# Kernel optimization log

Measured on AMD Instinct MI355X. Metric: run time of the kernel, lower is better.

## Reference

```python
import jax, jax.numpy as jnp
import numpy as np

V = 100000  # node_num
N = 2000000  # number of rows/messages
D = 64       # feature dim


def setup_inputs() -> dict:
    key = jax.random.key(0)
    k1, k2 = jax.random.split(key)
    H = jax.random.normal(k1, (N, D), dtype=jnp.float32)
    X_node = jax.random.randint(k2, (N,), 0, V, dtype=jnp.int64)
    return {"H": H, "X_node": X_node}


def reference(H, X_node):
    # Original builds a [V, N] one-hot mask (mask[v, n] = 1 iff X_node[n] == v)
    # and computes mask @ H. That is exactly a segment-sum of H rows by node id.
    return jax.ops.segment_sum(H, X_node, num_segments=V)  # [V, D]
```

## Files before the change

kernel.cpp:

```cpp
#include <hip/hip_runtime.h>


constexpr int D = 64;
constexpr int SCAN_TILE = 1024;

__global__ void hist_kernel(const int* __restrict__ idx, int* __restrict__ hist, int N) {
    int stride = gridDim.x * blockDim.x;
    for (int n = blockIdx.x * blockDim.x + threadIdx.x; n < N; n += stride)
        atomicAdd(&hist[idx[n]], 1);
}

__global__ __launch_bounds__(1024) void scan_tile_kernel(
    const int* __restrict__ hist, int* __restrict__ starts,
    int* __restrict__ tile_sums, int V)
{
    __shared__ int tmp[SCAN_TILE];
    int t = threadIdx.x;
    int v = blockIdx.x * SCAN_TILE + t;
    int x = (v < V) ? hist[v] : 0;
    tmp[t] = x;
    __syncthreads();
    for (int off = 1; off < SCAN_TILE; off <<= 1) {
        int y = (t >= off) ? tmp[t - off] : 0;
        __syncthreads();
        tmp[t] += y;
        __syncthreads();
    }
    if (v < V) starts[v] = tmp[t] - x;
    if (t == SCAN_TILE - 1) tile_sums[blockIdx.x] = tmp[t];
}

__global__ void scan_sums_kernel(int* tile_sums, int n_tiles) {
    if (threadIdx.x == 0 && blockIdx.x == 0) {
        int run = 0;
        for (int i = 0; i < n_tiles; ++i) { int s = tile_sums[i]; tile_sums[i] = run; run += s; }
    }
}

__global__ __launch_bounds__(1024) void scan_add_kernel(
    int* __restrict__ starts, const int* __restrict__ tile_sums, int V)
{
    int v = blockIdx.x * SCAN_TILE + threadIdx.x;
    if (v < V) starts[v] += tile_sums[blockIdx.x];
}

__global__ void scatter_kernel(const int* __restrict__ idx, int* __restrict__ cursor,
                               int* __restrict__ perm, int N)
{
    int stride = gridDim.x * blockDim.x;
    for (int n = blockIdx.x * blockDim.x + threadIdx.x; n < N; n += stride) {
        int node = idx[n];
        int pos = atomicAdd(&cursor[node], 1);
        perm[pos] = n;
    }
}

__global__ __launch_bounds__(256) void gather_kernel(
    const float* __restrict__ H, const int* __restrict__ perm,
    const int* __restrict__ starts, float* __restrict__ out, int V, int N)
{
    int wid  = blockIdx.x * (blockDim.x >> 6) + (threadIdx.x >> 6);
    int lane = threadIdx.x & 63;
    if (wid >= V) return;

    int beg = starts[wid];
    int end = (wid + 1 < V) ? starts[wid + 1] : N;
    int cnt = end - beg;

    float acc = 0.f;
    int base = 0;
    while (base < cnt) {
        int m = cnt - base; if (m > 64) m = 64;
        int n_l = (lane < m) ? perm[beg + base + lane] : 0;
        int i = 0;
        for (; i + 3 < m; i += 4) {
            int n0 = __shfl(n_l, i);
            int n1 = __shfl(n_l, i + 1);
            int n2 = __shfl(n_l, i + 2);
            int n3 = __shfl(n_l, i + 3);
            float a0 = H[(size_t)n0 * D + lane];
            float a1 = H[(size_t)n1 * D + lane];
            float a2 = H[(size_t)n2 * D + lane];
            float a3 = H[(size_t)n3 * D + lane];
            acc += a0; acc += a1; acc += a2; acc += a3;
        }
        for (; i < m; ++i) {
            int n = __shfl(n_l, i);
            acc += H[(size_t)n * D + lane];
        }
        base += m;
    }
    out[(size_t)wid * D + lane] = acc;
}

__global__ __launch_bounds__(256) void scatter_atomic_kernel(
    const float4* __restrict__ H4, const int* __restrict__ idx,
    float* __restrict__ out, int n_rows)
{
    long long t = (long long)blockIdx.x * blockDim.x + threadIdx.x;
    int n = (int)(t >> 4), q = (int)(t & 15);
    if (n >= n_rows) return;
    int node = idx[n];
    float4 v = H4[(size_t)n * 16 + q];
    float* o = out + (size_t)node * D + q * 4;
    atomicAdd(o + 0, v.x); atomicAdd(o + 1, v.y);
    atomicAdd(o + 2, v.z); atomicAdd(o + 3, v.w);
}

static inline size_t align_up(size_t x, size_t a) { return (x + a - 1) & ~(a - 1); }

extern "C" void kernel_launch(void* const* d_in, const int* in_sizes, int n_in,
                              void* d_out, int out_size, void* d_ws, size_t ws_size,
                              hipStream_t stream) {
    const float* H = (const float*)d_in[0];
    const int* idx = (const int*)d_in[1];
    float* out     = (float*)d_out;
    int N = in_sizes[1];
    int V = out_size / D;
    int n_tiles = (V + SCAN_TILE - 1) / SCAN_TILE;

    size_t off_perm  = 0;
    size_t off_hist  = align_up(off_perm + (size_t)N * 4, 256);
    size_t off_start = align_up(off_hist + (size_t)V * 4, 256);
    size_t off_cur   = align_up(off_start + (size_t)V * 4, 256);
    size_t off_tsum  = align_up(off_cur + (size_t)V * 4, 256);
    size_t need      = off_tsum + (size_t)n_tiles * 4;

    if (ws_size < need) {
        hipMemsetAsync(d_out, 0, (size_t)out_size * sizeof(float), stream);
        long long total = (long long)N * 16;
        scatter_atomic_kernel<<<(int)((total + 255) / 256), 256, 0, stream>>>(
            (const float4*)H, idx, out, N);
        return;
    }

    char* ws = (char*)d_ws;
    int* perm      = (int*)(ws + off_perm);
    int* hist      = (int*)(ws + off_hist);
    int* starts    = (int*)(ws + off_start);
    int* cursor    = (int*)(ws + off_cur);
    int* tile_sums = (int*)(ws + off_tsum);

    hipMemsetAsync(hist, 0, (size_t)V * 4, stream);

    hist_kernel<<<(N + 255) / 256, 256, 0, stream>>>(idx, hist, N);
    scan_tile_kernel<<<n_tiles, SCAN_TILE, 0, stream>>>(hist, starts, tile_sums, V);
    scan_sums_kernel<<<1, 64, 0, stream>>>(tile_sums, n_tiles);
    scan_add_kernel<<<n_tiles, SCAN_TILE, 0, stream>>>(starts, tile_sums, V);
    hipMemcpyAsync(cursor, starts, (size_t)V * 4, hipMemcpyDeviceToDevice, stream);
    scatter_kernel<<<(N + 255) / 256, 256, 0, stream>>>(idx, cursor, perm, N);

    int waves_per_block = 256 / 64;
    int grid = (V + waves_per_block - 1) / waves_per_block;
    gather_kernel<<<grid, 256, 0, stream>>>(H, perm, starts, out, V, N);
}
```

Before: 946.0 us.

## Replace per-node counting sort with coarse bucket partition and LDS accumulation

Replaces the full per-node histogram, multi-kernel scan and global-atomic scatter with a coarse bucketing pass. Rows go into buckets of 128 nodes using per-block LDS histograms, a column-wise scan of a blocks-by-buckets matrix, and an LDS-cursor partition that writes packed (node,row) pairs. Each accumulation block then sums its bucket's rows into an LDS tile with shared-memory atomics and writes the output once. This removes global atomics, the memset and memcpy, and the per-node wave imbalance. The cost is 8-byte permutation entries and LDS float atomics, and the partition is not stable within a bucket.

```diff
diff --git a/kernel.cpp b/kernel.cpp
--- a/kernel.cpp
+++ b/kernel.cpp
@@ -1,96 +1,136 @@
 #include <hip/hip_runtime.h>
 
 
-constexpr int D = 64;
-constexpr int SCAN_TILE = 1024;
+constexpr int D     = 64;
+constexpr int BHIST = 512;
+constexpr int NPB   = 128;
+constexpr int MAXC  = 1024;
 
-__global__ void hist_kernel(const int* __restrict__ idx, int* __restrict__ hist, int N) {
-    int stride = gridDim.x * blockDim.x;
-    for (int n = blockIdx.x * blockDim.x + threadIdx.x; n < N; n += stride)
-        atomicAdd(&hist[idx[n]], 1);
+__global__ __launch_bounds__(256) void bucket_hist_kernel(
+    const int* __restrict__ idx, int* __restrict__ matB, int N, int C)
+{
+    __shared__ int h[MAXC];
+    for (int c = threadIdx.x; c < C; c += blockDim.x) h[c] = 0;
+    __syncthreads();
+    int rpb = (N + BHIST - 1) / BHIST;
+    int lo = blockIdx.x * rpb;
+    int hi = lo + rpb; if (hi > N) hi = N;
+    for (int n = lo + threadIdx.x; n < hi; n += blockDim.x)
+        atomicAdd(&h[idx[n] >> 7], 1);
+    __syncthreads();
+    for (int c = threadIdx.x; c < C; c += blockDim.x)
+        matB[blockIdx.x * C + c] = h[c];
 }
 
-__global__ __launch_bounds__(1024) void scan_tile_kernel(
-    const int* __restrict__ hist, int* __restrict__ starts,
-    int* __restrict__ tile_sums, int V)
+__global__ __launch_bounds__(256) void scan_mat_kernel(
+    int* __restrict__ mat, int* __restrict__ colsum, int C)
 {
-    __shared__ int tmp[SCAN_TILE];
-    int t = threadIdx.x;
-    int v = blockIdx.x * SCAN_TILE + t;
-    int x = (v < V) ? hist[v] : 0;
-    tmp[t] = x;
-    __syncthreads();
-    for (int off = 1; off < SCAN_TILE; off <<= 1) {
-        int y = (t >= off) ? tmp[t - off] : 0;
-        __syncthreads();
-        tmp[t] += y;
-        __syncthreads();
+    int gw   = (blockIdx.x * blockDim.x + threadIdx.x) >> 6;
+    int lane = threadIdx.x & 63;
+    if (gw >= C) return;
+    int c = gw;
+    constexpr int VPL = BHIST / 64;
+    int v[VPL], p[VPL];
+    int run = 0;
+    #pragma unroll
+    for (int j = 0; j < VPL; ++j) {
+        v[j] = mat[(lane * VPL + j) * C + c];
+        p[j] = run;
+        run += v[j];
     }
-    if (v < V) starts[v] = tmp[t] - x;
-    if (t == SCAN_TILE - 1) tile_sums[blockIdx.x] = tmp[t];
+    int x = run;
+    #pragma unroll
+    for (int off = 1; off < 64; off <<= 1) {
+        int y = __shfl_up(x, off);
+        if (lane >= off) x += y;
+    }
+    int lane_excl = x - run;
+    #pragma unroll
+    for (int j = 0; j < VPL; ++j)
+        mat[(lane * VPL + j) * C + c] = lane_excl + p[j];
+    if (lane == 63) colsum[c] = x;
 }
 
-__global__ void scan_sums_kernel(int* tile_sums, int n_tiles) {
-    if (threadIdx.x == 0 && blockIdx.x == 0) {
-        int run = 0;
-        for (int i = 0; i < n_tiles; ++i) { int s = tile_sums[i]; tile_sums[i] = run; run += s; }
+__global__ __launch_bounds__(1024) void scan_cols_kernel(
+    const int* __restrict__ colsum, int* __restrict__ colbase, int C, int N)
+{
+    __shared__ int tmp[1024];
+    int t = threadIdx.x;
+    if (C <= 1024) {
+        int x = (t < C) ? colsum[t] : 0;
+        tmp[t] = x;
+        __syncthreads();
+        for (int off = 1; off < 1024; off <<= 1) {
+            int y = (t >= off) ? tmp[t - off] : 0;
+            __syncthreads();
+            tmp[t] += y;
+            __syncthreads();
+        }
+        if (t < C) colbase[t] = tmp[t] - x;
+        if (t == 0) colbase[C] = N;
+    } else {
+        if (t == 0) {
+            int run = 0;
+            for (int c = 0; c < C; ++c) { colbase[c] = run; run += colsum[c]; }
+            colbase[C] = run;
+        }
     }
 }
 
-__global__ __launch_bounds__(1024) void scan_add_kernel(
-    int* __restrict__ starts, const int* __restrict__ tile_sums, int V)
+__global__ __launch_bounds__(256) void partition_kernel(
+    const int* __restrict__ idx, const int* __restrict__ matP,
+    const int* __restrict__ colbase, long long* __restrict__ perm2,
+    int N, int C)
 {
-    int v = blockIdx.x * SCAN_TILE + threadIdx.x;
-    if (v < V) starts[v] += tile_sums[blockIdx.x];
-}
-
-__global__ void scatter_kernel(const int* __restrict__ idx, int* __restrict__ cursor,
-                               int* __restrict__ perm, int N)
-{
-    int stride = gridDim.x * blockDim.x;
-    for (int n = blockIdx.x * blockDim.x + threadIdx.x; n < N; n += stride) {
+    __shared__ int cur[MAXC];
+    for (int c = threadIdx.x; c < C; c += blockDim.x)
+        cur[c] = colbase[c] + matP[blockIdx.x * C + c];
+    __syncthreads();
+    int rpb = (N + BHIST - 1) / BHIST;
+    int lo = blockIdx.x * rpb;
+    int hi = lo + rpb; if (hi > N) hi = N;
+    for (int n = lo + threadIdx.x; n < hi; n += blockDim.x) {
         int node = idx[n];
-        int pos = atomicAdd(&cursor[node], 1);
-        perm[pos] = n;
+        int pos  = atomicAdd(&cur[node >> 7], 1);
+        long long pv = ((long long)node << 32) | (unsigned)n;
+        __builtin_nontemporal_store(pv, &perm2[pos]);
     }
 }
 
-__global__ __launch_bounds__(256) void gather_kernel(
-    const float* __restrict__ H, const int* __restrict__ perm,
-    const int* __restrict__ starts, float* __restrict__ out, int V, int N)
+__global__ __launch_bounds__(512) void accum_kernel(
+    const float* __restrict__ H, const long long* __restrict__ perm2,
+    const int* __restrict__ colbase, float* __restrict__ out, int V)
 {
-    int wid  = blockIdx.x * (blockDim.x >> 6) + (threadIdx.x >> 6);
-    int lane = threadIdx.x & 63;
-    if (wid >= V) return;
+    __shared__ float acc[NPB * D];
+    int tid = threadIdx.x;
+    for (int e = tid; e < NPB * D; e += 512) acc[e] = 0.f;
+    __syncthreads();
 
-    int beg = starts[wid];
-    int end = (wid + 1 < V) ? starts[wid + 1] : N;
-    int cnt = end - beg;
+    int c     = blockIdx.x;
+    int start = colbase[c];
+    int end   = colbase[c + 1];
+    int w     = tid >> 6;
+    int lane  = tid & 63;
 
-    float acc = 0.f;
-    int base = 0;
-    while (base < cnt) {
-        int m = cnt - base; if (m > 64) m = 64;
-        int n_l = (lane < m) ? perm[beg + base + lane] : 0;
-        int i = 0;
-        for (; i + 3 < m; i += 4) {
-            int n0 = __shfl(n_l, i);
-            int n1 = __shfl(n_l, i + 1);
-            int n2 = __shfl(n_l, i + 2);
-            int n3 = __shfl(n_l, i + 3);
-            float a0 = H[(size_t)n0 * D + lane];
-            float a1 = H[(size_t)n1 * D + lane];
-            float a2 = H[(size_t)n2 * D + lane];
-            float a3 = H[(size_t)n3 * D + lane];
-            acc += a0; acc += a1; acc += a2; acc += a3;
+    for (int r = start + w * 4; r < end; r += 32) {
+        #pragma unroll
+        for (int u = 0; u < 4; ++u) {
+            int rr = r + u;
+            if (rr < end) {
+                long long pv = perm2[rr];
+                int n     = (int)(pv & 0xffffffffLL);
+                int local = ((int)(pv >> 32)) & (NPB - 1);
+                float val = __builtin_nontemporal_load(&H[(size_t)n * D + lane]);
+                atomicAdd(&acc[local * D + lane], val);
+            }
         }
-        for (; i < m; ++i) {
-            int n = __shfl(n_l, i);
-            acc += H[(size_t)n * D + lane];
-        }
-        base += m;
     }
-    out[(size_t)wid * D + lane] = acc;
+    __syncthreads();
+
+    int vbase = c * NPB;
+    int nn = V - vbase; if (nn > NPB) nn = NPB;
+    for (int e = tid; e < nn * D; e += 512)
+        __builtin_nontemporal_store(acc[e], &out[(size_t)vbase * D + e]);
 }
 
 __global__ __launch_bounds__(256) void scatter_atomic_kernel(
@@ -117,16 +157,15 @@
     float* out     = (float*)d_out;
     int N = in_sizes[1];
     int V = out_size / D;
-    int n_tiles = (V + SCAN_TILE - 1) / SCAN_TILE;
+    int C = (V + NPB - 1) / NPB;
 
-    size_t off_perm  = 0;
-    size_t off_hist  = align_up(off_perm + (size_t)N * 4, 256);
-    size_t off_start = align_up(off_hist + (size_t)V * 4, 256);
-    size_t off_cur   = align_up(off_start + (size_t)V * 4, 256);
-    size_t off_tsum  = align_up(off_cur + (size_t)V * 4, 256);
-    size_t need      = off_tsum + (size_t)n_tiles * 4;
+    size_t off_mat   = 0;
+    size_t off_csum  = align_up(off_mat  + (size_t)BHIST * C * 4, 256);
+    size_t off_cbase = align_up(off_csum + (size_t)C * 4, 256);
+    size_t off_perm  = align_up(off_cbase + ((size_t)C + 1) * 4, 256);
+    size_t need      = off_perm + (size_t)N * 8;
 
-    if (ws_size < need) {
+    if (ws_size < need || C > MAXC) {
         hipMemsetAsync(d_out, 0, (size_t)out_size * sizeof(float), stream);
         long long total = (long long)N * 16;
         scatter_atomic_kernel<<<(int)((total + 255) / 256), 256, 0, stream>>>(
@@ -135,22 +174,14 @@
     }
 
     char* ws = (char*)d_ws;
-    int* perm      = (int*)(ws + off_perm);
-    int* hist      = (int*)(ws + off_hist);
-    int* starts    = (int*)(ws + off_start);
-    int* cursor    = (int*)(ws + off_cur);
-    int* tile_sums = (int*)(ws + off_tsum);
+    int* matB         = (int*)(ws + off_mat);
+    int* colsum       = (int*)(ws + off_csum);
+    int* colbase      = (int*)(ws + off_cbase);
+    long long* perm2  = (long long*)(ws + off_perm);
 
-    hipMemsetAsync(hist, 0, (size_t)V * 4, stream);
-
-    hist_kernel<<<(N + 255) / 256, 256, 0, stream>>>(idx, hist, N);
-    scan_tile_kernel<<<n_tiles, SCAN_TILE, 0, stream>>>(hist, starts, tile_sums, V);
-    scan_sums_kernel<<<1, 64, 0, stream>>>(tile_sums, n_tiles);
-    scan_add_kernel<<<n_tiles, SCAN_TILE, 0, stream>>>(starts, tile_sums, V);
-    hipMemcpyAsync(cursor, starts, (size_t)V * 4, hipMemcpyDeviceToDevice, stream);
-    scatter_kernel<<<(N + 255) / 256, 256, 0, stream>>>(idx, cursor, perm, N);
-
-    int waves_per_block = 256 / 64;
-    int grid = (V + waves_per_block - 1) / waves_per_block;
-    gather_kernel<<<grid, 256, 0, stream>>>(H, perm, starts, out, V, N);
+    bucket_hist_kernel<<<BHIST, 256, 0, stream>>>(idx, matB, N, C);
+    scan_mat_kernel<<<(C + 3) / 4, 256, 0, stream>>>(matB, colsum, C);
+    scan_cols_kernel<<<1, 1024, 0, stream>>>(colsum, colbase, C, N);
+    partition_kernel<<<BHIST, 256, 0, stream>>>(idx, matB, colbase, perm2, N, C);
+    accum_kernel<<<C, 512, 0, stream>>>(H, perm2, colbase, out, V);
 }
```

Result: slower. 1.498 ms (+58.4%).
